# Kernel optimization log

Measured on AMD Instinct MI355X. Metric: run time of the kernel, lower is better.

Reference implementation:

```python
import jax, jax.numpy as jnp
import numpy as np

N_NODES = 50000
N_EDGES = 1000000
F = 256          # feature_size
NC = 300         # n_content_dims
ED = 64          # embedding_dim = 2**int(log2(F/4))
L = 3            # n_layers


def setup_inputs() -> dict:
    key = jax.random.key(0)
    ks = jax.random.split(key, 20)
    s = 0.05  # weight init scale
    return {
        'node_ids': jnp.arange(N_NODES, dtype=jnp.int32),
        'content': jax.random.normal(ks[0], (N_NODES, NC), jnp.float32),
        'src': jax.random.randint(ks[1], (N_EDGES,), 0, N_NODES, jnp.int32),
        'dst': jax.random.randint(ks[2], (N_EDGES,), 0, N_NODES, jnp.int32),
        'emb': jax.random.normal(ks[3], (N_NODES + 1, ED), jnp.float32) / ED,
        'W_exp': jax.random.normal(ks[4], (F, ED), jnp.float32) * s,
        'b_exp': jnp.zeros((F,), jnp.float32),
        'W_p1': jax.random.normal(ks[5], (NC, NC), jnp.float32) * s,
        'b_p1': jnp.zeros((NC,), jnp.float32),
        'W_p2': jax.random.normal(ks[6], (F, NC), jnp.float32) * s,
        'b_p2': jnp.zeros((F,), jnp.float32),
        'W_conv': jax.random.normal(ks[7], (L, F, 2 * F), jnp.float32) * s,
        'b_conv': jnp.zeros((L, F), jnp.float32),
        'Wo1': jax.random.normal(ks[8], (L - 1, F, F), jnp.float32) * s,
        'bo1': jnp.zeros((L - 1, F), jnp.float32),
        'Wo2': jax.random.normal(ks[9], (L - 1, F, F), jnp.float32) * s,
        'bo2': jnp.zeros((L - 1, F), jnp.float32),
    }


def _lrelu(x):
    return jax.nn.leaky_relu(x, 0.1)


def reference(node_ids, content, src, dst, emb, W_exp, b_exp, W_p1, b_p1,
              W_p2, b_p2, W_conv, b_conv, Wo1, bo1, Wo2, bo2):
    # initial node repr: expansion(node_emb) + proj(content)  (GaussianNoise = identity at eval)
    h = _lrelu(emb[node_ids] @ W_exp.T + b_exp)                 # [N, F]
    c = _lrelu(content @ W_p1.T + b_p1)
    c = _lrelu(c @ W_p2.T + b_p2)
    h = h + c

    ones = jnp.ones((src.shape[0],), h.dtype)
    deg = jax.ops.segment_sum(ones, dst, num_segments=N_NODES)  # in-degree
    w = (deg + 1.0)[:, None]                                    # +1 for self-loop

    for i in range(L):
        # message passing: sum neighbor h (with self-loop), then neighbor mean
        agg = jax.ops.segment_sum(h[src], dst, num_segments=N_NODES) + h  # [N, F]
        h_agg = (agg - h) / jnp.maximum(w - 1.0, 1.0)
        h_concat = jnp.concatenate([h, h_agg], axis=1)          # [N, 2F]
        h_new = h_concat @ W_conv[i].T + b_conv[i]
        if i < L - 1:
            h_new = _lrelu(h_new)
        # L2-normalize rows
        h_new = h_new / jnp.maximum(
            jnp.linalg.norm(h_new, axis=1, keepdims=True), 1e-6)
        if i < L - 1:  # W_out block (non-prediction layers)
            h_new = _lrelu(h_new @ Wo1[i].T + bo1[i])
            h_new = h_new @ Wo2[i].T + bo2[i]
        h = h_new
    return h
```

## Files before the change

### kernel.cpp

```cpp
#include <hip/hip_runtime.h>
#include <stdint.h>

#define NNODES 50000
#define NROWS_PAD 50048
#define NEDGES 1000000
#define FD 256
#define NCPAD 384
#define EDIM 64
#define NSCAN ((NNODES + 255) / 256)

typedef unsigned short u16;
typedef __attribute__((ext_vector_type(8))) short short8;
typedef __attribute__((ext_vector_type(4))) float floatx4;

__device__ __forceinline__ float bf2f(u16 x) {
    union { unsigned u; float f; } c; c.u = ((unsigned)x) << 16; return c.f;
}
__device__ __forceinline__ u16 f2bf(float f) {
    union { float f; unsigned u; } c; c.f = f;
    unsigned u = c.u;
    return (u16)((u + 0x7fffu + ((u >> 16) & 1u)) >> 16);
}
__device__ __forceinline__ void gload16(const u16* g, u16* l) {
    __builtin_amdgcn_global_load_lds(
        (const __attribute__((address_space(1))) void*)g,
        (__attribute__((address_space(3))) void*)l, 16, 0, 0);
}

__global__ void detect_kernel(const u16* p, int* flag) {
    __shared__ int smax;
    if (threadIdx.x == 0) smax = 0;
    __syncthreads();
    int m = 0;
    for (int i = threadIdx.x; i < 8192; i += 256) {
        int e = (p[i] >> 7) & 0xFF;
        m = m > e ? m : e;
    }
    atomicMax(&smax, m);
    __syncthreads();
    if (threadIdx.x == 0) *flag = (smax >= 140) ? 1 : 0;
}

__global__ void convert_kernel(u16* arena, const int* flagp,
    const void* wexp, const void* bexp, const void* wp1, const void* bp1,
    const void* wp2, const void* bp2, const void* wconv, const void* bconv,
    const void* wo1, const void* bo1, const void* wo2, const void* bo2)
{
    const int offs[13]  = {0,16384,16640,164096,164480,262784,263040,
                           656256,657024,788096,788608,919680,920192};
    const int rreal[12] = {256,1,300,1,256,1,768,1,512,1,512,1};
    const int creal[12] = {64,256,300,300,300,256,512,768,256,512,256,512};
    const int cpad[12]  = {64,256,384,384,384,256,512,768,256,512,256,512};
    long gid = (long)blockIdx.x * 256 + threadIdx.x;
    if (gid >= 920192) return;
    const void* srcs[12] = {wexp,bexp,wp1,bp1,wp2,bp2,wconv,bconv,wo1,bo1,wo2,bo2};
    int fl = *flagp;
    int t = 0;
    #pragma unroll
    for (int i = 1; i < 12; ++i) if (gid >= offs[i]) t = i;
    long local = gid - offs[t];
    int r = (int)(local / cpad[t]);
    int c = (int)(local % cpad[t]);
    u16 v = 0;
    if (r < rreal[t] && c < creal[t]) {
        long si = (long)r * creal[t] + c;
        v = fl ? f2bf(((const float*)srcs[t])[si]) : ((const u16*)srcs[t])[si];
    }
    arena[gid] = v;
}

template<int CP>
__global__ void pad2d_kernel(u16* dst, const void* src, int rows_real,
                             int cols_real, long total, const int* flagp)
{
    long gid = (long)blockIdx.x * 256 + threadIdx.x;
    if (gid >= total) return;
    int r = (int)(gid / CP);
    int c = (int)(gid % CP);
    u16 v = 0;
    if (r < rows_real && c < cols_real) {
        long si = (long)r * cols_real + c;
        v = (*flagp) ? f2bf(((const float*)src)[si]) : ((const u16*)src)[si];
    }
    dst[gid] = v;
}

__global__ void count_kernel(const int* dst, int* deg) {
    int e = blockIdx.x * blockDim.x + threadIdx.x;
    if (e < NEDGES) atomicAdd(&deg[dst[e]], 1);
}

__global__ __launch_bounds__(256) void scan1_kernel(const int* deg, int* bsum) {
    __shared__ int s[256];
    int t = threadIdx.x;
    int i = blockIdx.x * 256 + t;
    s[t] = (i < NNODES) ? deg[i] : 0;
    __syncthreads();
    #pragma unroll
    for (int off = 128; off > 0; off >>= 1) {
        if (t < off) s[t] += s[t + off];
        __syncthreads();
    }
    if (t == 0) bsum[blockIdx.x] = s[0];
}

__global__ __launch_bounds__(256) void scan2_kernel(int* bsum, int* row_start) {
    __shared__ int s[256];
    int t = threadIdx.x;
    int v = (t < NSCAN) ? bsum[t] : 0;
    s[t] = v;
    __syncthreads();
    for (int off = 1; off < 256; off <<= 1) {
        int x = (t >= off) ? s[t - off] : 0;
        __syncthreads();
        s[t] += x;
        __syncthreads();
    }
    if (t < NSCAN) bsum[t] = s[t] - v;
    if (t == 0) row_start[NNODES] = NEDGES;
}

__global__ __launch_bounds__(256) void scan3_kernel(const int* deg, const int* bsum,
        int* row_start, int* cursor, float* inv_w) {
    __shared__ int s[256];
    int t = threadIdx.x;
    int i = blockIdx.x * 256 + t;
    int v = (i < NNODES) ? deg[i] : 0;
    s[t] = v;
    __syncthreads();
    for (int off = 1; off < 256; off <<= 1) {
        int x = (t >= off) ? s[t - off] : 0;
        __syncthreads();
        s[t] += x;
        __syncthreads();
    }
    if (i < NNODES) {
        int base = bsum[blockIdx.x] + s[t] - v;
        row_start[i] = base;
        cursor[i] = base;
        inv_w[i] = 1.0f / (float)(v > 0 ? v : 1);
    }
}

__global__ void fill_kernel(const int* src, const int* dst, int* cursor, int* esrc) {
    int e = blockIdx.x * blockDim.x + threadIdx.x;
    if (e < NEDGES) {
        int v = dst[e];
        int pos = atomicAdd(&cursor[v], 1);
        if ((unsigned)pos < (unsigned)NEDGES) esrc[pos] = src[e];
    }
}

__global__ __launch_bounds__(256) void gemm128_kernel(
    const u16* A, const u16* A2, int KA, int lda,
    const u16* W, int ldw, const u16* bias,
    u16* out, float* outf, int ldo, const u16* addsrc,
    int M, int N, int K, int act)
{
    __shared__ __align__(16) u16 sA[2][128 * 32];
    __shared__ __align__(16) u16 sB[2][128 * 32];
    const int t = threadIdx.x;
    const int wave = t >> 6, lane = t & 63;
    const int quad = lane >> 4, l16 = lane & 15;
    const int wm = wave >> 1, wn = wave & 1;
    const int bm = blockIdx.y * 128, bn = blockIdx.x * 128;
    const int lrow = lane >> 2;
    const int lcol = (lane & 3) * 8;

    floatx4 acc[4][4];
    #pragma unroll
    for (int i = 0; i < 4; ++i)
        #pragma unroll
        for (int j = 0; j < 4; ++j) acc[i][j] = (floatx4){0.f, 0.f, 0.f, 0.f};

    for (int kt = 0; kt < K; kt += 64) {
        const u16* Ap = A; int kk = kt;
        if (A2 != nullptr && kt >= KA) { Ap = A2; kk = kt - KA; }
        #pragma unroll
        for (int h = 0; h < 2; ++h) {
            #pragma unroll
            for (int c = 0; c < 2; ++c) {
                int r = wave * 32 + c * 16;
                gload16(Ap + (size_t)(bm + r + lrow) * lda + kk + h * 32 + lcol,
                        &sA[h][r * 32]);
            }
        }
        #pragma unroll
        for (int h = 0; h < 2; ++h) {
            #pragma unroll
            for (int c = 0; c < 2; ++c) {
                int r = wave * 32 + c * 16;
                gload16(W + (size_t)(bn + r + lrow) * ldw + kt + h * 32 + lcol,
                        &sB[h][r * 32]);
            }
        }
        __syncthreads();
        #pragma unroll
        for (int h = 0; h < 2; ++h) {
            short8 af[4], bf[4];
            #pragma unroll
            for (int mt = 0; mt < 4; ++mt)
                af[mt] = *(const short8*)&sA[h][(wm * 64 + mt * 16 + l16) * 32 + quad * 8];
            #pragma unroll
            for (int nt = 0; nt < 4; ++nt)
                bf[nt] = *(const short8*)&sB[h][(wn * 64 + nt * 16 + l16) * 32 + quad * 8];
            #pragma unroll
            for (int mt = 0; mt < 4; ++mt)
                #pragma unroll
                for (int nt = 0; nt < 4; ++nt)
                    acc[mt][nt] = __builtin_amdgcn_mfma_f32_16x16x32_bf16(af[mt], bf[nt], acc[mt][nt], 0, 0, 0);
        }
        __syncthreads();
    }

    #pragma unroll
    for (int nt = 0; nt < 4; ++nt) {
        int gn = bn + wn * 64 + nt * 16 + l16;
        float bv = (bias != nullptr) ? bf2f(bias[gn]) : 0.0f;
        #pragma unroll
        for (int mt = 0; mt < 4; ++mt) {
            #pragma unroll
            for (int r = 0; r < 4; ++r) {
                int gm = bm + wm * 64 + mt * 16 + quad * 4 + r;
                if (gm < M) {
                    float v = acc[mt][nt][r] + bv;
                    if (act) v = v > 0.0f ? v : 0.1f * v;
                    if (addsrc != nullptr) v += bf2f(addsrc[(size_t)gm * ldo + gn]);
                    if (outf != nullptr) outf[(size_t)gm * ldo + gn] = v;
                    else out[(size_t)gm * ldo + gn] = f2bf(v);
                }
            }
        }
    }
}

__global__ __launch_bounds__(512, 4) void layer_kernel(
    const u16* __restrict__ h, const u16* __restrict__ agg,
    const u16* __restrict__ Wc, const u16* __restrict__ bc,
    const u16* __restrict__ W1, const u16* __restrict__ b1,
    const u16* __restrict__ W2, const u16* __restrict__ b2,
    u16* __restrict__ out)
{
    __shared__ __align__(16) u16 sA[2][64 * 32];
    __shared__ __align__(16) u16 sB[2][256 * 32];
    __shared__ __align__(16) u16 T[64 * 256];

    const int t = threadIdx.x;
    const int wave = t >> 6, lane = t & 63;
    const int quad = lane >> 4, l16 = lane & 15;
    const int wm = wave >> 2, wn = wave & 3;
    const int lrow = lane >> 2, lcol = (lane & 3) * 8;
    const int bm = blockIdx.x * 64;

    floatx4 acc[2][4];
    #pragma unroll
    for (int i = 0; i < 2; ++i)
        #pragma unroll
        for (int j = 0; j < 4; ++j) acc[i][j] = (floatx4){0.f, 0.f, 0.f, 0.f};

    for (int kt = 0; kt < 512; kt += 64) {
        const u16* Ap = (kt < 256) ? h : agg;
        const int kk = kt & 255;
        {
            int hh = wave & 1, r0 = (wave >> 1) * 16;
            gload16(Ap + (size_t)(bm + r0 + lrow) * 256 + kk + hh * 32 + lcol,
                    &sA[hh][r0 * 32]);
        }
        #pragma unroll
        for (int c = 0; c < 4; ++c) {
            int hh = c >> 1, r0 = wave * 32 + (c & 1) * 16;
            gload16(Wc + (size_t)(r0 + lrow) * 512 + kt + hh * 32 + lcol,
                    &sB[hh][r0 * 32]);
        }
        __syncthreads();
        #pragma unroll
        for (int g = 0; g < 2; ++g) {
            short8 af[2], bf[4];
            #pragma unroll
            for (int mt = 0; mt < 2; ++mt)
                af[mt] = *(const short8*)&sA[g][(wm * 32 + mt * 16 + l16) * 32 + quad * 8];
            #pragma unroll
            for (int nt = 0; nt < 4; ++nt)
                bf[nt] = *(const short8*)&sB[g][(wn * 64 + nt * 16 + l16) * 32 + quad * 8];
            #pragma unroll
            for (int mt = 0; mt < 2; ++mt)
                #pragma unroll
                for (int nt = 0; nt < 4; ++nt)
                    acc[mt][nt] = __builtin_amdgcn_mfma_f32_16x16x32_bf16(af[mt], bf[nt], acc[mt][nt], 0, 0, 0);
        }
        __syncthreads();
    }
    #pragma unroll
    for (int nt = 0; nt < 4; ++nt) {
        int col = wn * 64 + nt * 16 + l16;
        float bv = bf2f(bc[col]);
        #pragma unroll
        for (int mt = 0; mt < 2; ++mt) {
            #pragma unroll
            for (int r = 0; r < 4; ++r) {
                int row = wm * 32 + mt * 16 + quad * 4 + r;
                float v = acc[mt][nt][r] + bv;
                v = v > 0.f ? v : 0.1f * v;
                T[(row * 256 + col) ^ ((row & 7) << 3)] = f2bf(v);
            }
        }
    }
    __syncthreads();

    #pragma unroll
    for (int rr = 0; rr < 8; ++rr) {
        int row = wave * 8 + rr;
        int idx = (row * 256 + lane * 4) ^ ((row & 7) << 3);
        ushort4 tv = *(const ushort4*)&T[idx];
        float x0 = bf2f(tv.x), x1 = bf2f(tv.y), x2 = bf2f(tv.z), x3 = bf2f(tv.w);
        float ss = x0 * x0 + x1 * x1 + x2 * x2 + x3 * x3;
        #pragma unroll
        for (int off = 32; off > 0; off >>= 1) ss += __shfl_xor(ss, off);
        float s = 1.0f / fmaxf(sqrtf(ss), 1e-6f);
        ushort4 ov;
        ov.x = f2bf(x0 * s); ov.y = f2bf(x1 * s);
        ov.z = f2bf(x2 * s); ov.w = f2bf(x3 * s);
        *(ushort4*)&T[idx] = ov;
    }
    __syncthreads();

    #pragma unroll
    for (int i = 0; i < 2; ++i)
        #pragma unroll
        for (int j = 0; j < 4; ++j) acc[i][j] = (floatx4){0.f, 0.f, 0.f, 0.f};
    for (int kt = 0; kt < 256; kt += 64) {
        #pragma unroll
        for (int c = 0; c < 4; ++c) {
            int hh = c >> 1, r0 = wave * 32 + (c & 1) * 16;
            gload16(W1 + (size_t)(r0 + lrow) * 256 + kt + hh * 32 + lcol,
                    &sB[hh][r0 * 32]);
        }
        __syncthreads();
        #pragma unroll
        for (int g = 0; g < 2; ++g) {
            short8 af[2], bf[4];
            #pragma unroll
            for (int mt = 0; mt < 2; ++mt) {
                int row = wm * 32 + mt * 16 + l16;
                af[mt] = *(const short8*)&T[(row * 256 + kt + g * 32 + quad * 8) ^ ((row & 7) << 3)];
            }
            #pragma unroll
            for (int nt = 0; nt < 4; ++nt)
                bf[nt] = *(const short8*)&sB[g][(wn * 64 + nt * 16 + l16) * 32 + quad * 8];
            #pragma unroll
            for (int mt = 0; mt < 2; ++mt)
                #pragma unroll
                for (int nt = 0; nt < 4; ++nt)
                    acc[mt][nt] = __builtin_amdgcn_mfma_f32_16x16x32_bf16(af[mt], bf[nt], acc[mt][nt], 0, 0, 0);
        }
        __syncthreads();
    }
    #pragma unroll
    for (int nt = 0; nt < 4; ++nt) {
        int col = wn * 64 + nt * 16 + l16;
        float bv = bf2f(b1[col]);
        #pragma unroll
        for (int mt = 0; mt < 2; ++mt) {
            #pragma unroll
            for (int r = 0; r < 4; ++r) {
                int row = wm * 32 + mt * 16 + quad * 4 + r;
                float v = acc[mt][nt][r] + bv;
                v = v > 0.f ? v : 0.1f * v;
                T[(row * 256 + col) ^ ((row & 7) << 3)] = f2bf(v);
            }
        }
    }
    __syncthreads();

    #pragma unroll
    for (int i = 0; i < 2; ++i)
        #pragma unroll
        for (int j = 0; j < 4; ++j) acc[i][j] = (floatx4){0.f, 0.f, 0.f, 0.f};
    for (int kt = 0; kt < 256; kt += 64) {
        #pragma unroll
        for (int c = 0; c < 4; ++c) {
            int hh = c >> 1, r0 = wave * 32 + (c & 1) * 16;
            gload16(W2 + (size_t)(r0 + lrow) * 256 + kt + hh * 32 + lcol,
                    &sB[hh][r0 * 32]);
        }
        __syncthreads();
        #pragma unroll
        for (int g = 0; g < 2; ++g) {
            short8 af[2], bf[4];
            #pragma unroll
            for (int mt = 0; mt < 2; ++mt) {
                int row = wm * 32 + mt * 16 + l16;
                af[mt] = *(const short8*)&T[(row * 256 + kt + g * 32 + quad * 8) ^ ((row & 7) << 3)];
            }
            #pragma unroll
            for (int nt = 0; nt < 4; ++nt)
                bf[nt] = *(const short8*)&sB[g][(wn * 64 + nt * 16 + l16) * 32 + quad * 8];
            #pragma unroll
            for (int mt = 0; mt < 2; ++mt)
                #pragma unroll
                for (int nt = 0; nt < 4; ++nt)
                    acc[mt][nt] = __builtin_amdgcn_mfma_f32_16x16x32_bf16(af[mt], bf[nt], acc[mt][nt], 0, 0, 0);
        }
        __syncthreads();
    }
    #pragma unroll
    for (int nt = 0; nt < 4; ++nt) {
        int col = wn * 64 + nt * 16 + l16;
        float bv = bf2f(b2[col]);
        #pragma unroll
        for (int mt = 0; mt < 2; ++mt) {
            #pragma unroll
            for (int r = 0; r < 4; ++r) {
                int row = wm * 32 + mt * 16 + quad * 4 + r;
                int gm = bm + row;
                if (gm < NNODES) {
                    float v = acc[mt][nt][r] + bv;
                    out[(size_t)gm * 256 + col] = f2bf(v);
                }
            }
        }
    }
}

__global__ __launch_bounds__(256) void agg_kernel(
    const u16* h, const int* row_start, const int* esrc,
    const float* inv_w, u16* out)
{
    int gid = blockIdx.x * blockDim.x + threadIdx.x;
    int wid = gid >> 6;
    int lane = gid & 63;
    if (wid >= NNODES) return;
    int e0 = row_start[wid], e1 = row_start[wid + 1];
    e0 = max(0, min(e0, NEDGES));
    e1 = max(e0, min(e1, NEDGES));
    float a0 = 0.f, a1 = 0.f, a2 = 0.f, a3 = 0.f;
    int e = e0;
    for (; e + 4 <= e1; e += 4) {
        int u0 = esrc[e + 0]; if ((unsigned)u0 >= (unsigned)NNODES) u0 = 0;
        int u1 = esrc[e + 1]; if ((unsigned)u1 >= (unsigned)NNODES) u1 = 0;
        int u2 = esrc[e + 2]; if ((unsigned)u2 >= (unsigned)NNODES) u2 = 0;
        int u3 = esrc[e + 3]; if ((unsigned)u3 >= (unsigned)NNODES) u3 = 0;
        ushort4 t0 = *(const ushort4*)(h + (size_t)u0 * FD + lane * 4);
        ushort4 t1 = *(const ushort4*)(h + (size_t)u1 * FD + lane * 4);
        ushort4 t2 = *(const ushort4*)(h + (size_t)u2 * FD + lane * 4);
        ushort4 t3 = *(const ushort4*)(h + (size_t)u3 * FD + lane * 4);
        a0 += bf2f(t0.x) + bf2f(t1.x) + bf2f(t2.x) + bf2f(t3.x);
        a1 += bf2f(t0.y) + bf2f(t1.y) + bf2f(t2.y) + bf2f(t3.y);
        a2 += bf2f(t0.z) + bf2f(t1.z) + bf2f(t2.z) + bf2f(t3.z);
        a3 += bf2f(t0.w) + bf2f(t1.w) + bf2f(t2.w) + bf2f(t3.w);
    }
    for (; e < e1; ++e) {
        int u = esrc[e];
        if ((unsigned)u >= (unsigned)NNODES) u = 0;
        ushort4 tv = *(const ushort4*)(h + (size_t)u * FD + lane * 4);
        a0 += bf2f(tv.x); a1 += bf2f(tv.y); a2 += bf2f(tv.z); a3 += bf2f(tv.w);
    }
    float s = inv_w[wid];
    ushort4 ov;
    ov.x = f2bf(a0 * s); ov.y = f2bf(a1 * s); ov.z = f2bf(a2 * s); ov.w = f2bf(a3 * s);
    *(ushort4*)(out + (size_t)wid * FD + lane * 4) = ov;
}

__global__ __launch_bounds__(256) void norm_kernel(const u16* in, u16* out, int act)
{
    int gid = blockIdx.x * blockDim.x + threadIdx.x;
    int wid = gid >> 6, lane = gid & 63;
    if (wid >= NNODES) return;
    ushort4 tv = *(const ushort4*)(in + (size_t)wid * FD + lane * 4);
    u16 raw[4] = {tv.x, tv.y, tv.z, tv.w};
    float f[4]; float ss = 0.f;
    #pragma unroll
    for (int j = 0; j < 4; ++j) {
        float x = bf2f(raw[j]);
        if (act) x = x > 0.f ? x : 0.1f * x;
        f[j] = x; ss += x * x;
    }
    #pragma unroll
    for (int off = 32; off > 0; off >>= 1) ss += __shfl_xor(ss, off);
    float s = 1.0f / fmaxf(sqrtf(ss), 1e-6f);
    ushort4 ov;
    ov.x = f2bf(f[0] * s); ov.y = f2bf(f[1] * s);
    ov.z = f2bf(f[2] * s); ov.w = f2bf(f[3] * s);
    *(ushort4*)(out + (size_t)wid * FD + lane * 4) = ov;
}

__global__ __launch_bounds__(256) void normf_kernel(float* io)
{
    int gid = blockIdx.x * blockDim.x + threadIdx.x;
    int wid = gid >> 6, lane = gid & 63;
    if (wid >= NNODES) return;
    float4 v = *(float4*)(io + (size_t)wid * FD + lane * 4);
    float ss = v.x * v.x + v.y * v.y + v.z * v.z + v.w * v.w;
    #pragma unroll
    for (int off = 32; off > 0; off >>= 1) ss += __shfl_xor(ss, off);
    float s = 1.0f / fmaxf(sqrtf(ss), 1e-6f);
    v.x *= s; v.y *= s; v.z *= s; v.w *= s;
    *(float4*)(io + (size_t)wid * FD + lane * 4) = v;
}

extern "C" void kernel_launch(void* const* d_in, const int* in_sizes, int n_in,
                              void* d_out, int out_size, void* d_ws, size_t ws_size,
                              hipStream_t stream) {
    const void* content = d_in[1];
    const int* src      = (const int*)d_in[2];
    const int* dst      = (const int*)d_in[3];
    const void* emb     = d_in[4];

    char* ws = (char*)d_ws;
    u16* arena = (u16*)(ws);
    u16* hbuf  = (u16*)(ws + 1840640);
    u16* buf2  = (u16*)(ws + 27465216);
    u16* cpad  = (u16*)(ws + 27465216);
    u16* ebuf  = (u16*)(ws + 65902336);
    int*   deg    = (int*)(ws + 78714368);
    int*   rs     = (int*)(ws + 78914560);
    int*   cursor = (int*)(ws + 79114752);
    float* inv_w  = (float*)(ws + 79314944);
    int*   esrc   = (int*)(ws + 79515136);
    int*   bsum   = (int*)(ws + 83515648);
    int*   flag   = (int*)(ws + 83516672);
    u16* cbuf  = (u16*)d_out;

    u16* aWexp  = arena;            u16* aBexp  = arena + 16384;
    u16* aWp1   = arena + 16640;    u16* aBp1   = arena + 164096;
    u16* aWp2   = arena + 164480;   u16* aBp2   = arena + 262784;
    u16* aWconv = arena + 263040;   u16* aBconv = arena + 656256;
    u16* aWo1   = arena + 657024;   u16* aBo1   = arena + 788096;
    u16* aWo2   = arena + 788608;   u16* aBo2   = arena + 919680;

    const int MB128 = NROWS_PAD / 128;
    const int MB64  = NROWS_PAD / 64;
    dim3 blk(256);

    detect_kernel<<<1, 256, 0, stream>>>((const u16*)content, flag);
    convert_kernel<<<(920192 + 255) / 256, 256, 0, stream>>>(arena, flag,
        d_in[5], d_in[6], d_in[7], d_in[8], d_in[9], d_in[10], d_in[11],
        d_in[12], d_in[13], d_in[14], d_in[15], d_in[16]);
    {
        long tot_c = (long)NROWS_PAD * NCPAD;
        pad2d_kernel<NCPAD><<<(int)((tot_c + 255) / 256), 256, 0, stream>>>(
            cpad, content, NNODES, 300, tot_c, flag);
        long tot_e = (long)NROWS_PAD * EDIM;
        pad2d_kernel<EDIM><<<(int)((tot_e + 255) / 256), 256, 0, stream>>>(
            ebuf, emb, NNODES, EDIM, tot_e, flag);
    }

    gemm128_kernel<<<dim3(2, MB128), blk, 0, stream>>>(ebuf, nullptr, 0, EDIM,
        aWexp, EDIM, aBexp, hbuf, nullptr, FD, nullptr, NNODES, FD, EDIM, 1);
    gemm128_kernel<<<dim3(3, MB128), blk, 0, stream>>>(cpad, nullptr, 0, NCPAD,
        aWp1, NCPAD, aBp1, cbuf, nullptr, NCPAD, nullptr, NNODES, NCPAD, NCPAD, 1);
    gemm128_kernel<<<dim3(2, MB128), blk, 0, stream>>>(cbuf, nullptr, 0, NCPAD,
        aWp2, NCPAD, aBp2, hbuf, nullptr, FD, hbuf, NNODES, FD, NCPAD, 1);

    hipMemsetAsync(deg, 0, (size_t)NNODES * 4, stream);
    count_kernel<<<(NEDGES + 255) / 256, 256, 0, stream>>>(dst, deg);
    scan1_kernel<<<NSCAN, 256, 0, stream>>>(deg, bsum);
    scan2_kernel<<<1, 256, 0, stream>>>(bsum, rs);
    scan3_kernel<<<NSCAN, 256, 0, stream>>>(deg, bsum, rs, cursor, inv_w);
    fill_kernel<<<(NEDGES + 255) / 256, 256, 0, stream>>>(src, dst, cursor, esrc);

    for (int i = 0; i < 3; ++i) {
        agg_kernel<<<(NNODES * 64) / 256, blk, 0, stream>>>(hbuf, rs, esrc, inv_w, buf2);
        if (i < 2) {
            layer_kernel<<<dim3(MB64), dim3(512), 0, stream>>>(
                hbuf, buf2,
                aWconv + (size_t)i * FD * 2 * FD, aBconv + (size_t)i * FD,
                aWo1 + (size_t)i * FD * FD, aBo1 + (size_t)i * FD,
                aWo2 + (size_t)i * FD * FD, aBo2 + (size_t)i * FD,
                hbuf);
        } else {
            gemm128_kernel<<<dim3(2, MB128), blk, 0, stream>>>(hbuf, buf2, FD, FD,
                aWconv + (size_t)i * FD * 2 * FD, 2 * FD, aBconv + (size_t)i * FD,
                nullptr, (float*)d_out, FD, nullptr, NNODES, FD, 2 * FD, 0);
            normf_kernel<<<(NNODES * 64) / 256, blk, 0, stream>>>((float*)d_out);
        }
    }
}
```

Baseline: 804.8 us.

## Fuse prep/count, init GEMMs with CSR fill, and final GEMM with normalization

Merges the weight/content/embedding conversion kernels and the degree count into one interleaved prep kernel. Fuses the three initial projection GEMMs into a single per-tile kernel that keeps the intermediate content activation in LDS, and interleaves the CSR fill blocks into the same grid. The layer kernel now computes row norms from register partial sums instead of a separate LDS pass. A dedicated final kernel fuses the last conv GEMM with L2 normalization. This removes launches and the global round-trips for intermediates, at the cost of large LDS use per block and mixed block roles that may hurt occupancy.

Measured after the change: 688.3 us. 14.5% less time.

```diff
diff --git a/kernel.cpp b/kernel.cpp
--- a/kernel.cpp
+++ b/kernel.cpp
@@ -41,53 +41,71 @@
     if (threadIdx.x == 0) *flag = (smax >= 140) ? 1 : 0;
 }
 
-__global__ void convert_kernel(u16* arena, const int* flagp,
+#define NB_CONV 1798
+#define NB_PADC 37536
+#define NB_PADE 6256
+#define NB_CNT  1954
+#define NB_OTH  (NB_CONV + NB_PADC + NB_PADE)
+#define PREP_GRID 47572
+__global__ __launch_bounds__(512) void prep_kernel(
+    u16* arena, const int* flagp,
     const void* wexp, const void* bexp, const void* wp1, const void* bp1,
     const void* wp2, const void* bp2, const void* wconv, const void* bconv,
-    const void* wo1, const void* bo1, const void* wo2, const void* bo2)
+    const void* wo1, const void* bo1, const void* wo2, const void* bo2,
+    u16* cpad, const void* content, u16* ebuf, const void* emb,
+    const int* dst, int* deg)
 {
-    const int offs[13]  = {0,16384,16640,164096,164480,262784,263040,
-                           656256,657024,788096,788608,919680,920192};
-    const int rreal[12] = {256,1,300,1,256,1,768,1,512,1,512,1};
-    const int creal[12] = {64,256,300,300,300,256,512,768,256,512,256,512};
-    const int cpad[12]  = {64,256,384,384,384,256,512,768,256,512,256,512};
-    long gid = (long)blockIdx.x * 256 + threadIdx.x;
-    if (gid >= 920192) return;
-    const void* srcs[12] = {wexp,bexp,wp1,bp1,wp2,bp2,wconv,bconv,wo1,bo1,wo2,bo2};
+    const int bid = blockIdx.x;
+    const int q = bid / 24, r = bid % 24;
+    if (r == 23) {
+        if (q >= NB_CNT) return;
+        int e = q * 512 + threadIdx.x;
+        if (e < NEDGES) atomicAdd(&deg[dst[e]], 1);
+        return;
+    }
+    long oid = (long)q * 23 + r;
+    if (oid >= NB_OTH) return;
     int fl = *flagp;
-    int t = 0;
-    #pragma unroll
-    for (int i = 1; i < 12; ++i) if (gid >= offs[i]) t = i;
-    long local = gid - offs[t];
-    int r = (int)(local / cpad[t]);
-    int c = (int)(local % cpad[t]);
-    u16 v = 0;
-    if (r < rreal[t] && c < creal[t]) {
-        long si = (long)r * creal[t] + c;
-        v = fl ? f2bf(((const float*)srcs[t])[si]) : ((const u16*)srcs[t])[si];
-    }
-    arena[gid] = v;
-}
-
-template<int CP>
-__global__ void pad2d_kernel(u16* dst, const void* src, int rows_real,
-                             int cols_real, long total, const int* flagp)
-{
-    long gid = (long)blockIdx.x * 256 + threadIdx.x;
-    if (gid >= total) return;
-    int r = (int)(gid / CP);
-    int c = (int)(gid % CP);
-    u16 v = 0;
-    if (r < rows_real && c < cols_real) {
-        long si = (long)r * cols_real + c;
-        v = (*flagp) ? f2bf(((const float*)src)[si]) : ((const u16*)src)[si];
-    }
-    dst[gid] = v;
-}
-
-__global__ void count_kernel(const int* dst, int* deg) {
-    int e = blockIdx.x * blockDim.x + threadIdx.x;
-    if (e < NEDGES) atomicAdd(&deg[dst[e]], 1);
+    if (oid < NB_CONV) {
+        const int offs[13]  = {0,16384,16640,164096,164480,262784,263040,
+                               656256,657024,788096,788608,919680,920192};
+        const int rreal[12] = {256,1,300,1,256,1,768,1,512,1,512,1};
+        const int creal[12] = {64,256,300,300,300,256,512,768,256,512,256,512};
+        const int cpd[12]   = {64,256,384,384,384,256,512,768,256,512,256,512};
+        long gid = oid * 512 + threadIdx.x;
+        if (gid >= 920192) return;
+        const void* srcs[12] = {wexp,bexp,wp1,bp1,wp2,bp2,wconv,bconv,wo1,bo1,wo2,bo2};
+        int t = 0;
+        #pragma unroll
+        for (int i = 1; i < 12; ++i) if (gid >= offs[i]) t = i;
+        long local = gid - offs[t];
+        int rr = (int)(local / cpd[t]);
+        int cc = (int)(local % cpd[t]);
+        u16 v = 0;
+        if (rr < rreal[t] && cc < creal[t]) {
+            long si = (long)rr * creal[t] + cc;
+            v = fl ? f2bf(((const float*)srcs[t])[si]) : ((const u16*)srcs[t])[si];
+        }
+        arena[gid] = v;
+    } else if (oid < NB_CONV + NB_PADC) {
+        long gid = (oid - NB_CONV) * 512 + threadIdx.x;
+        int rr = (int)(gid / NCPAD), cc = (int)(gid % NCPAD);
+        u16 v = 0;
+        if (rr < NNODES && cc < 300) {
+            long si = (long)rr * 300 + cc;
+            v = fl ? f2bf(((const float*)content)[si]) : ((const u16*)content)[si];
+        }
+        cpad[gid] = v;
+    } else {
+        long gid = (oid - NB_CONV - NB_PADC) * 512 + threadIdx.x;
+        int rr = (int)(gid / EDIM), cc = (int)(gid % EDIM);
+        u16 v = 0;
+        if (rr < NNODES) {
+            long si = (long)rr * EDIM + cc;
+            v = fl ? f2bf(((const float*)emb)[si]) : ((const u16*)emb)[si];
+        }
+        ebuf[gid] = v;
+    }
 }
 
 __global__ __launch_bounds__(256) void scan1_kernel(const int* deg, int* bsum) {
@@ -142,95 +160,152 @@
     }
 }
 
-__global__ void fill_kernel(const int* src, const int* dst, int* cursor, int* esrc) {
-    int e = blockIdx.x * blockDim.x + threadIdx.x;
-    if (e < NEDGES) {
-        int v = dst[e];
-        int pos = atomicAdd(&cursor[v], 1);
-        if ((unsigned)pos < (unsigned)NEDGES) esrc[pos] = src[e];
-    }
-}
-
-__global__ __launch_bounds__(256) void gemm128_kernel(
-    const u16* A, const u16* A2, int KA, int lda,
-    const u16* W, int ldw, const u16* bias,
-    u16* out, float* outf, int ldo, const u16* addsrc,
-    int M, int N, int K, int act)
+#define IF_GRID (391 * 7)
+__global__ __launch_bounds__(512, 4) void initfill_kernel(
+    const u16* __restrict__ cpad, const u16* __restrict__ ebuf,
+    const u16* __restrict__ Wp1, const u16* __restrict__ bp1,
+    const u16* __restrict__ Wp2, const u16* __restrict__ bp2,
+    const u16* __restrict__ Wexp, const u16* __restrict__ bexp,
+    u16* __restrict__ hbuf,
+    const int* __restrict__ src, const int* __restrict__ dst,
+    int* __restrict__ cursor, int* __restrict__ esrc)
 {
-    __shared__ __align__(16) u16 sA[2][128 * 32];
-    __shared__ __align__(16) u16 sB[2][128 * 32];
+    __shared__ __align__(16) u16 sA[64 * 32];
+    __shared__ __align__(16) u16 sB[384 * 32];
+    __shared__ __align__(16) u16 T[64 * 384];
+
+    const int g7 = blockIdx.x / 7, r7 = blockIdx.x % 7;
+    if (r7 >= 2) {
+        int fb = g7 * 5 + (r7 - 2);
+        int e = fb * 512 + threadIdx.x;
+        if (e < NEDGES) {
+            int v = dst[e];
+            int pos = atomicAdd(&cursor[v], 1);
+            if ((unsigned)pos < (unsigned)NEDGES) esrc[pos] = src[e];
+        }
+        return;
+    }
+    const int bm = (g7 * 2 + r7) * 64;
     const int t = threadIdx.x;
     const int wave = t >> 6, lane = t & 63;
     const int quad = lane >> 4, l16 = lane & 15;
-    const int wm = wave >> 1, wn = wave & 1;
-    const int bm = blockIdx.y * 128, bn = blockIdx.x * 128;
-    const int lrow = lane >> 2;
-    const int lcol = (lane & 3) * 8;
-
-    floatx4 acc[4][4];
-    #pragma unroll
-    for (int i = 0; i < 4; ++i)
-        #pragma unroll
-        for (int j = 0; j < 4; ++j) acc[i][j] = (floatx4){0.f, 0.f, 0.f, 0.f};
-
-    for (int kt = 0; kt < K; kt += 64) {
-        const u16* Ap = A; int kk = kt;
-        if (A2 != nullptr && kt >= KA) { Ap = A2; kk = kt - KA; }
-        #pragma unroll
-        for (int h = 0; h < 2; ++h) {
-            #pragma unroll
-            for (int c = 0; c < 2; ++c) {
-                int r = wave * 32 + c * 16;
-                gload16(Ap + (size_t)(bm + r + lrow) * lda + kk + h * 32 + lcol,
-                        &sA[h][r * 32]);
-            }
-        }
-        #pragma unroll
-        for (int h = 0; h < 2; ++h) {
-            #pragma unroll
-            for (int c = 0; c < 2; ++c) {
-                int r = wave * 32 + c * 16;
-                gload16(W + (size_t)(bn + r + lrow) * ldw + kt + h * 32 + lcol,
-                        &sB[h][r * 32]);
-            }
-        }
-        __syncthreads();
-        #pragma unroll
-        for (int h = 0; h < 2; ++h) {
-            short8 af[4], bf[4];
-            #pragma unroll
-            for (int mt = 0; mt < 4; ++mt)
-                af[mt] = *(const short8*)&sA[h][(wm * 64 + mt * 16 + l16) * 32 + quad * 8];
-            #pragma unroll
-            for (int nt = 0; nt < 4; ++nt)
-                bf[nt] = *(const short8*)&sB[h][(wn * 64 + nt * 16 + l16) * 32 + quad * 8];
-            #pragma unroll
-            for (int mt = 0; mt < 4; ++mt)
-                #pragma unroll
-                for (int nt = 0; nt < 4; ++nt)
-                    acc[mt][nt] = __builtin_amdgcn_mfma_f32_16x16x32_bf16(af[mt], bf[nt], acc[mt][nt], 0, 0, 0);
+    const int wm = wave >> 2, wn = wave & 3;
+    const int lrow = lane >> 2, lcol = (lane & 3) * 8;
+
+    floatx4 a1[2][6];
+    #pragma unroll
+    for (int i = 0; i < 2; ++i)
+        #pragma unroll
+        for (int j = 0; j < 6; ++j) a1[i][j] = (floatx4){0.f, 0.f, 0.f, 0.f};
+    for (int kt = 0; kt < 384; kt += 32) {
+        if (wave < 4)
+            gload16(cpad + (size_t)(bm + wave * 16 + lrow) * NCPAD + kt + lcol,
+                    &sA[(wave * 16) * 32]);
+        #pragma unroll
+        for (int c = 0; c < 3; ++c) {
+            int r0 = wave * 48 + c * 16;
+            gload16(Wp1 + (size_t)(r0 + lrow) * NCPAD + kt + lcol, &sB[r0 * 32]);
+        }
+        __syncthreads();
+        short8 af[2];
+        #pragma unroll
+        for (int mt = 0; mt < 2; ++mt)
+            af[mt] = *(const short8*)&sA[(wm * 32 + mt * 16 + l16) * 32 + quad * 8];
+        #pragma unroll
+        for (int nt = 0; nt < 6; ++nt) {
+            short8 bf = *(const short8*)&sB[(wn * 96 + nt * 16 + l16) * 32 + quad * 8];
+            a1[0][nt] = __builtin_amdgcn_mfma_f32_16x16x32_bf16(af[0], bf, a1[0][nt], 0, 0, 0);
+            a1[1][nt] = __builtin_amdgcn_mfma_f32_16x16x32_bf16(af[1], bf, a1[1][nt], 0, 0, 0);
+        }
+        __syncthreads();
+    }
+    #pragma unroll
+    for (int nt = 0; nt < 6; ++nt) {
+        int col = wn * 96 + nt * 16 + l16;
+        float bv = bf2f(bp1[col]);
+        #pragma unroll
+        for (int mt = 0; mt < 2; ++mt)
+            #pragma unroll
+            for (int rr = 0; rr < 4; ++rr) {
+                int row = wm * 32 + mt * 16 + quad * 4 + rr;
+                float v = a1[mt][nt][rr] + bv;
+                v = v > 0.f ? v : 0.1f * v;
+                T[(row * NCPAD + col) ^ ((row & 7) << 3)] = f2bf(v);
+            }
+    }
+    __syncthreads();
+
+    floatx4 a2[2][4];
+    #pragma unroll
+    for (int i = 0; i < 2; ++i)
+        #pragma unroll
+        for (int j = 0; j < 4; ++j) a2[i][j] = (floatx4){0.f, 0.f, 0.f, 0.f};
+    for (int kt = 0; kt < 384; kt += 32) {
+        #pragma unroll
+        for (int c = 0; c < 2; ++c) {
+            int r0 = wave * 32 + c * 16;
+            gload16(Wp2 + (size_t)(r0 + lrow) * NCPAD + kt + lcol, &sB[r0 * 32]);
+        }
+        __syncthreads();
+        short8 af[2];
+        #pragma unroll
+        for (int mt = 0; mt < 2; ++mt) {
+            int row = wm * 32 + mt * 16 + l16;
+            af[mt] = *(const short8*)&T[(row * NCPAD + kt + quad * 8) ^ ((row & 7) << 3)];
+        }
+        #pragma unroll
+        for (int nt = 0; nt < 4; ++nt) {
+            short8 bf = *(const short8*)&sB[(wn * 64 + nt * 16 + l16) * 32 + quad * 8];
+            a2[0][nt] = __builtin_amdgcn_mfma_f32_16x16x32_bf16(af[0], bf, a2[0][nt], 0, 0, 0);
+            a2[1][nt] = __builtin_amdgcn_mfma_f32_16x16x32_bf16(af[1], bf, a2[1][nt], 0, 0, 0);
+        }
+        __syncthreads();
+    }
+
+    floatx4 aE[2][4];
+    #pragma unroll
+    for (int i = 0; i < 2; ++i)
+        #pragma unroll
+        for (int j = 0; j < 4; ++j) aE[i][j] = (floatx4){0.f, 0.f, 0.f, 0.f};
+    for (int kt = 0; kt < 64; kt += 32) {
+        if (wave < 4)
+            gload16(ebuf + (size_t)(bm + wave * 16 + lrow) * EDIM + kt + lcol,
+                    &sA[(wave * 16) * 32]);
+        #pragma unroll
+        for (int c = 0; c < 2; ++c) {
+            int r0 = wave * 32 + c * 16;
+            gload16(Wexp + (size_t)(r0 + lrow) * EDIM + kt + lcol, &sB[r0 * 32]);
+        }
+        __syncthreads();
+        short8 af[2];
+        #pragma unroll
+        for (int mt = 0; mt < 2; ++mt)
+            af[mt] = *(const short8*)&sA[(wm * 32 + mt * 16 + l16) * 32 + quad * 8];
+        #pragma unroll
+        for (int nt = 0; nt < 4; ++nt) {
+            short8 bf = *(const short8*)&sB[(wn * 64 + nt * 16 + l16) * 32 + quad * 8];
+            aE[0][nt] = __builtin_amdgcn_mfma_f32_16x16x32_bf16(af[0], bf, aE[0][nt], 0, 0, 0);
+            aE[1][nt] = __builtin_amdgcn_mfma_f32_16x16x32_bf16(af[1], bf, aE[1][nt], 0, 0, 0);
         }
         __syncthreads();
     }
 
     #pragma unroll
     for (int nt = 0; nt < 4; ++nt) {
-        int gn = bn + wn * 64 + nt * 16 + l16;
-        float bv = (bias != nullptr) ? bf2f(bias[gn]) : 0.0f;
-        #pragma unroll
-        for (int mt = 0; mt < 4; ++mt) {
-            #pragma unroll
-            for (int r = 0; r < 4; ++r) {
-                int gm = bm + wm * 64 + mt * 16 + quad * 4 + r;
-                if (gm < M) {
-                    float v = acc[mt][nt][r] + bv;
-                    if (act) v = v > 0.0f ? v : 0.1f * v;
-                    if (addsrc != nullptr) v += bf2f(addsrc[(size_t)gm * ldo + gn]);
-                    if (outf != nullptr) outf[(size_t)gm * ldo + gn] = v;
-                    else out[(size_t)gm * ldo + gn] = f2bf(v);
+        int col = wn * 64 + nt * 16 + l16;
+        float bE = bf2f(bexp[col]), b2 = bf2f(bp2[col]);
+        #pragma unroll
+        for (int mt = 0; mt < 2; ++mt)
+            #pragma unroll
+            for (int rr = 0; rr < 4; ++rr) {
+                int row = wm * 32 + mt * 16 + quad * 4 + rr;
+                int gm = bm + row;
+                if (gm < NNODES) {
+                    float hE = aE[mt][nt][rr] + bE; hE = hE > 0.f ? hE : 0.1f * hE;
+                    float c2 = a2[mt][nt][rr] + b2; c2 = c2 > 0.f ? c2 : 0.1f * c2;
+                    hbuf[(size_t)gm * FD + col] = f2bf(hE + c2);
                 }
             }
-        }
     }
 }
 
@@ -244,6 +319,7 @@
     __shared__ __align__(16) u16 sA[2][64 * 32];
     __shared__ __align__(16) u16 sB[2][256 * 32];
     __shared__ __align__(16) u16 T[64 * 256];
+    __shared__ float ssq[4][64];
 
     const int t = threadIdx.x;
     const int wave = t >> 6, lane = t & 63;
@@ -290,39 +366,55 @@
         }
         __syncthreads();
     }
-    #pragma unroll
-    for (int nt = 0; nt < 4; ++nt) {
-        int col = wn * 64 + nt * 16 + l16;
-        float bv = bf2f(bc[col]);
-        #pragma unroll
-        for (int mt = 0; mt < 2; ++mt) {
-            #pragma unroll
-            for (int r = 0; r < 4; ++r) {
-                int row = wm * 32 + mt * 16 + quad * 4 + r;
-                float v = acc[mt][nt][r] + bv;
-                v = v > 0.f ? v : 0.1f * v;
-                T[(row * 256 + col) ^ ((row & 7) << 3)] = f2bf(v);
-            }
-        }
-    }
-    __syncthreads();
-
-    #pragma unroll
-    for (int rr = 0; rr < 8; ++rr) {
-        int row = wave * 8 + rr;
-        int idx = (row * 256 + lane * 4) ^ ((row & 7) << 3);
-        ushort4 tv = *(const ushort4*)&T[idx];
-        float x0 = bf2f(tv.x), x1 = bf2f(tv.y), x2 = bf2f(tv.z), x3 = bf2f(tv.w);
-        float ss = x0 * x0 + x1 * x1 + x2 * x2 + x3 * x3;
-        #pragma unroll
-        for (int off = 32; off > 0; off >>= 1) ss += __shfl_xor(ss, off);
-        float s = 1.0f / fmaxf(sqrtf(ss), 1e-6f);
-        ushort4 ov;
-        ov.x = f2bf(x0 * s); ov.y = f2bf(x1 * s);
-        ov.z = f2bf(x2 * s); ov.w = f2bf(x3 * s);
-        *(ushort4*)&T[idx] = ov;
-    }
-    __syncthreads();
+    {
+        float part[2][4];
+        #pragma unroll
+        for (int mt = 0; mt < 2; ++mt)
+            #pragma unroll
+            for (int rr = 0; rr < 4; ++rr) part[mt][rr] = 0.f;
+        #pragma unroll
+        for (int nt = 0; nt < 4; ++nt) {
+            float bv = bf2f(bc[wn * 64 + nt * 16 + l16]);
+            #pragma unroll
+            for (int mt = 0; mt < 2; ++mt)
+                #pragma unroll
+                for (int rr = 0; rr < 4; ++rr) {
+                    float v = acc[mt][nt][rr] + bv;
+                    v = v > 0.f ? v : 0.1f * v;
+                    part[mt][rr] += v * v;
+                }
+        }
+        #pragma unroll
+        for (int off = 1; off < 16; off <<= 1)
+            #pragma unroll
+            for (int mt = 0; mt < 2; ++mt)
+                #pragma unroll
+                for (int rr = 0; rr < 4; ++rr)
+                    part[mt][rr] += __shfl_xor(part[mt][rr], off);
+        if (l16 == 0)
+            #pragma unroll
+            for (int mt = 0; mt < 2; ++mt)
+                #pragma unroll
+                for (int rr = 0; rr < 4; ++rr)
+                    ssq[wn][wm * 32 + mt * 16 + quad * 4 + rr] = part[mt][rr];
+        __syncthreads();
+        #pragma unroll
+        for (int mt = 0; mt < 2; ++mt)
+            #pragma unroll
+            for (int rr = 0; rr < 4; ++rr) {
+                int row = wm * 32 + mt * 16 + quad * 4 + rr;
+                float s = 1.0f / fmaxf(sqrtf(ssq[0][row] + ssq[1][row] +
+                                             ssq[2][row] + ssq[3][row]), 1e-6f);
+                #pragma unroll
+                for (int nt = 0; nt < 4; ++nt) {
+                    int col = wn * 64 + nt * 16 + l16;
+                    float v = acc[mt][nt][rr] + bf2f(bc[col]);
+                    v = v > 0.f ? v : 0.1f * v;
+                    T[(row * 256 + col) ^ ((row & 7) << 3)] = f2bf(v * s);
+                }
+            }
+        __syncthreads();
+    }
 
     #pragma unroll
     for (int i = 0; i < 2; ++i)
@@ -420,6 +512,108 @@
             }
         }
     }
+}
+
+__global__ __launch_bounds__(512, 4) void final_kernel(
+    const u16* __restrict__ h, const u16* __restrict__ agg,
+    const u16* __restrict__ Wc, const u16* __restrict__ bc,
+    float* __restrict__ out)
+{
+    __shared__ __align__(16) u16 sA[2][64 * 32];
+    __shared__ __align__(16) u16 sB[2][256 * 32];
+    __shared__ float ssq[4][64];
+
+    const int t = threadIdx.x;
+    const int wave = t >> 6, lane = t & 63;
+    const int quad = lane >> 4, l16 = lane & 15;
+    const int wm = wave >> 2, wn = wave & 3;
+    const int lrow = lane >> 2, lcol = (lane & 3) * 8;
+    const int bm = blockIdx.x * 64;
+
+    floatx4 acc[2][4];
+    #pragma unroll
+    for (int i = 0; i < 2; ++i)
+        #pragma unroll
+        for (int j = 0; j < 4; ++j) acc[i][j] = (floatx4){0.f, 0.f, 0.f, 0.f};
+
+    for (int kt = 0; kt < 512; kt += 64) {
+        const u16* Ap = (kt < 256) ? h : agg;
+        const int kk = kt & 255;
+        {
+            int hh = wave & 1, r0 = (wave >> 1) * 16;
+            gload16(Ap + (size_t)(bm + r0 + lrow) * 256 + kk + hh * 32 + lcol,
+                    &sA[hh][r0 * 32]);
+        }
+        #pragma unroll
+        for (int c = 0; c < 4; ++c) {
+            int hh = c >> 1, r0 = wave * 32 + (c & 1) * 16;
+            gload16(Wc + (size_t)(r0 + lrow) * 512 + kt + hh * 32 + lcol,
+                    &sB[hh][r0 * 32]);
+        }
+        __syncthreads();
+        #pragma unroll
+        for (int g = 0; g < 2; ++g) {
+            short8 af[2], bf[4];
+            #pragma unroll
+            for (int mt = 0; mt < 2; ++mt)
+                af[mt] = *(const short8*)&sA[g][(wm * 32 + mt * 16 + l16) * 32 + quad * 8];
+            #pragma unroll
+            for (int nt = 0; nt < 4; ++nt)
+                bf[nt] = *(const short8*)&sB[g][(wn * 64 + nt * 16 + l16) * 32 + quad * 8];
+            #pragma unroll
+            for (int mt = 0; mt < 2; ++mt)
+                #pragma unroll
+                for (int nt = 0; nt < 4; ++nt)
+                    acc[mt][nt] = __builtin_amdgcn_mfma_f32_16x16x32_bf16(af[mt], bf[nt], acc[mt][nt], 0, 0, 0);
+        }
+        __syncthreads();
+    }
+    float part[2][4];
+    #pragma unroll
+    for (int mt = 0; mt < 2; ++mt)
+        #pragma unroll
+        for (int rr = 0; rr < 4; ++rr) part[mt][rr] = 0.f;
+    #pragma unroll
+    for (int nt = 0; nt < 4; ++nt) {
+        float bv = bf2f(bc[wn * 64 + nt * 16 + l16]);
+        #pragma unroll
+        for (int mt = 0; mt < 2; ++mt)
+            #pragma unroll
+            for (int rr = 0; rr < 4; ++rr) {
+                float v = acc[mt][nt][rr] + bv;
+                part[mt][rr] += v * v;
+            }
+    }
+    #pragma unroll
+    for (int off = 1; off < 16; off <<= 1)
+        #pragma unroll
+        for (int mt = 0; mt < 2; ++mt)
+            #pragma unroll
+            for (int rr = 0; rr < 4; ++rr)
+                part[mt][rr] += __shfl_xor(part[mt][rr], off);
+    if (l16 == 0)
+        #pragma unroll
+        for (int mt = 0; mt < 2; ++mt)
+            #pragma unroll
+            for (int rr = 0; rr < 4; ++rr)
+                ssq[wn][wm * 32 + mt * 16 + quad * 4 + rr] = part[mt][rr];
+    __syncthreads();
+    #pragma unroll
+    for (int mt = 0; mt < 2; ++mt)
+        #pragma unroll
+        for (int rr = 0; rr < 4; ++rr) {
+            int row = wm * 32 + mt * 16 + quad * 4 + rr;
+            int gm = bm + row;
+            float s = 1.0f / fmaxf(sqrtf(ssq[0][row] + ssq[1][row] +
+                                         ssq[2][row] + ssq[3][row]), 1e-6f);
+            if (gm < NNODES) {
+                #pragma unroll
+                for (int nt = 0; nt < 4; ++nt) {
+                    int col = wn * 64 + nt * 16 + l16;
+                    out[(size_t)gm * 256 + col] = (acc[mt][nt][rr] + bf2f(bc[col])) * s;
+                }
+            }
+        }
 }
 
 __global__ __launch_bounds__(256) void agg_kernel(
@@ -461,43 +655,6 @@
     *(ushort4*)(out + (size_t)wid * FD + lane * 4) = ov;
 }
 
-__global__ __launch_bounds__(256) void norm_kernel(const u16* in, u16* out, int act)
-{
-    int gid = blockIdx.x * blockDim.x + threadIdx.x;
-    int wid = gid >> 6, lane = gid & 63;
-    if (wid >= NNODES) return;
-    ushort4 tv = *(const ushort4*)(in + (size_t)wid * FD + lane * 4);
-    u16 raw[4] = {tv.x, tv.y, tv.z, tv.w};
-    float f[4]; float ss = 0.f;
-    #pragma unroll
-    for (int j = 0; j < 4; ++j) {
-        float x = bf2f(raw[j]);
-        if (act) x = x > 0.f ? x : 0.1f * x;
-        f[j] = x; ss += x * x;
-    }
-    #pragma unroll
-    for (int off = 32; off > 0; off >>= 1) ss += __shfl_xor(ss, off);
-    float s = 1.0f / fmaxf(sqrtf(ss), 1e-6f);
-    ushort4 ov;
-    ov.x = f2bf(f[0] * s); ov.y = f2bf(f[1] * s);
-    ov.z = f2bf(f[2] * s); ov.w = f2bf(f[3] * s);
-    *(ushort4*)(out + (size_t)wid * FD + lane * 4) = ov;
-}
-
-__global__ __launch_bounds__(256) void normf_kernel(float* io)
-{
-    int gid = blockIdx.x * blockDim.x + threadIdx.x;
-    int wid = gid >> 6, lane = gid & 63;
-    if (wid >= NNODES) return;
-    float4 v = *(float4*)(io + (size_t)wid * FD + lane * 4);
-    float ss = v.x * v.x + v.y * v.y + v.z * v.z + v.w * v.w;
-    #pragma unroll
-    for (int off = 32; off > 0; off >>= 1) ss += __shfl_xor(ss, off);
-    float s = 1.0f / fmaxf(sqrtf(ss), 1e-6f);
-    v.x *= s; v.y *= s; v.z *= s; v.w *= s;
-    *(float4*)(io + (size_t)wid * FD + lane * 4) = v;
-}
-
 extern "C" void kernel_launch(void* const* d_in, const int* in_sizes, int n_in,
                               void* d_out, int out_size, void* d_ws, size_t ws_size,
                               hipStream_t stream) {
@@ -519,7 +676,6 @@
     int*   esrc   = (int*)(ws + 79515136);
     int*   bsum   = (int*)(ws + 83515648);
     int*   flag   = (int*)(ws + 83516672);
-    u16* cbuf  = (u16*)d_out;
 
     u16* aWexp  = arena;            u16* aBexp  = arena + 16384;
     u16* aWp1   = arena + 16640;    u16* aBp1   = arena + 164096;
@@ -528,39 +684,24 @@
     u16* aWo1   = arena + 657024;   u16* aBo1   = arena + 788096;
     u16* aWo2   = arena + 788608;   u16* aBo2   = arena + 919680;
 
-    const int MB128 = NROWS_PAD / 128;
-    const int MB64  = NROWS_PAD / 64;
-    dim3 blk(256);
+    const int MB64 = NROWS_PAD / 64;
 
     detect_kernel<<<1, 256, 0, stream>>>((const u16*)content, flag);
-    convert_kernel<<<(920192 + 255) / 256, 256, 0, stream>>>(arena, flag,
+    hipMemsetAsync(deg, 0, (size_t)NNODES * 4, stream);
+    prep_kernel<<<PREP_GRID, 512, 0, stream>>>(arena, flag,
         d_in[5], d_in[6], d_in[7], d_in[8], d_in[9], d_in[10], d_in[11],
-        d_in[12], d_in[13], d_in[14], d_in[15], d_in[16]);
-    {
-        long tot_c = (long)NROWS_PAD * NCPAD;
-        pad2d_kernel<NCPAD><<<(int)((tot_c + 255) / 256), 256, 0, stream>>>(
-            cpad, content, NNODES, 300, tot_c, flag);
-        long tot_e = (long)NROWS_PAD * EDIM;
-        pad2d_kernel<EDIM><<<(int)((tot_e + 255) / 256), 256, 0, stream>>>(
-            ebuf, emb, NNODES, EDIM, tot_e, flag);
-    }
-
-    gemm128_kernel<<<dim3(2, MB128), blk, 0, stream>>>(ebuf, nullptr, 0, EDIM,
-        aWexp, EDIM, aBexp, hbuf, nullptr, FD, nullptr, NNODES, FD, EDIM, 1);
-    gemm128_kernel<<<dim3(3, MB128), blk, 0, stream>>>(cpad, nullptr, 0, NCPAD,
-        aWp1, NCPAD, aBp1, cbuf, nullptr, NCPAD, nullptr, NNODES, NCPAD, NCPAD, 1);
-    gemm128_kernel<<<dim3(2, MB128), blk, 0, stream>>>(cbuf, nullptr, 0, NCPAD,
-        aWp2, NCPAD, aBp2, hbuf, nullptr, FD, hbuf, NNODES, FD, NCPAD, 1);
-
-    hipMemsetAsync(deg, 0, (size_t)NNODES * 4, stream);
-    count_kernel<<<(NEDGES + 255) / 256, 256, 0, stream>>>(dst, deg);
+        d_in[12], d_in[13], d_in[14], d_in[15], d_in[16],
+        cpad, content, ebuf, emb, dst, deg);
+
     scan1_kernel<<<NSCAN, 256, 0, stream>>>(deg, bsum);
     scan2_kernel<<<1, 256, 0, stream>>>(bsum, rs);
     scan3_kernel<<<NSCAN, 256, 0, stream>>>(deg, bsum, rs, cursor, inv_w);
-    fill_kernel<<<(NEDGES + 255) / 256, 256, 0, stream>>>(src, dst, cursor, esrc);
+
+    initfill_kernel<<<IF_GRID, 512, 0, stream>>>(cpad, ebuf,
+        aWp1, aBp1, aWp2, aBp2, aWexp, aBexp, hbuf, src, dst, cursor, esrc);
 
     for (int i = 0; i < 3; ++i) {
-        agg_kernel<<<(NNODES * 64) / 256, blk, 0, stream>>>(hbuf, rs, esrc, inv_w, buf2);
+        agg_kernel<<<(NNODES * 64) / 256, 256, 0, stream>>>(hbuf, rs, esrc, inv_w, buf2);
         if (i < 2) {
             layer_kernel<<<dim3(MB64), dim3(512), 0, stream>>>(
                 hbuf, buf2,
@@ -569,10 +710,10 @@
                 aWo2 + (size_t)i * FD * FD, aBo2 + (size_t)i * FD,
                 hbuf);
         } else {
-            gemm128_kernel<<<dim3(2, MB128), blk, 0, stream>>>(hbuf, buf2, FD, FD,
-                aWconv + (size_t)i * FD * 2 * FD, 2 * FD, aBconv + (size_t)i * FD,
-                nullptr, (float*)d_out, FD, nullptr, NNODES, FD, 2 * FD, 0);
-            normf_kernel<<<(NNODES * 64) / 256, blk, 0, stream>>>((float*)d_out);
-        }
-    }
-}
+            final_kernel<<<dim3(MB64), dim3(512), 0, stream>>>(
+                hbuf, buf2,
+                aWconv + (size_t)i * FD * 2 * FD, aBconv + (size_t)i * FD,
+                (float*)d_out);
+        }
+    }
+}
```
